# Optimization experiments

Hardware: AMD Instinct MI355X
Metric: run time of the kernel (lower is better)

## Reference

```python
import jax, jax.numpy as jnp
import numpy as np

DIM = 1024
NUM_HEADS = 16
HEAD_DIM = DIM // NUM_HEADS
MLP_DIM = 4 * DIM
EPS = 1e-5


def layer_norm(x, g, b):
    mu = jnp.mean(x, axis=-1, keepdims=True)
    var = jnp.mean(jnp.square(x - mu), axis=-1, keepdims=True)
    return (x - mu) * jax.lax.rsqrt(var + EPS) * g + b


def setup_inputs() -> dict:
    key = jax.random.key(0)
    ks = jax.random.split(key, 12)
    B, L = 2, 2048
    s = lambda n: 1.0 / np.sqrt(n)
    return {
        "x": jax.random.normal(ks[0], (B, L, DIM), jnp.float32),
        "attn_mask": jnp.tril(jnp.ones((L, L), jnp.int32))[None, None],  # [1,1,L,L]
        "w_qkv": jax.random.normal(ks[1], (DIM, 3 * DIM), jnp.float32) * s(DIM),
        "b_qkv": jnp.zeros((3 * DIM,), jnp.float32),
        "w_proj": jax.random.normal(ks[2], (DIM, DIM), jnp.float32) * s(DIM),
        "b_proj": jnp.zeros((DIM,), jnp.float32),
        "w_fc1": jax.random.normal(ks[3], (DIM, MLP_DIM), jnp.float32) * s(DIM),
        "b_fc1": jnp.zeros((MLP_DIM,), jnp.float32),
        "w_fc2": jax.random.normal(ks[4], (MLP_DIM, DIM), jnp.float32) * s(MLP_DIM),
        "b_fc2": jnp.zeros((DIM,), jnp.float32),
        "g1": jnp.ones((DIM,), jnp.float32),
        "beta1": jnp.zeros((DIM,), jnp.float32),
        "g2": jnp.ones((DIM,), jnp.float32),
        "beta2": jnp.zeros((DIM,), jnp.float32),
    }


def reference(x, attn_mask, w_qkv, b_qkv, w_proj, b_proj, w_fc1, b_fc1,
              w_fc2, b_fc2, g1, beta1, g2, beta2):
    B, L, D = x.shape
    scale = HEAD_DIM ** -0.5

    # --- attention branch (pre-norm) ---
    h = layer_norm(x, g1, beta1)
    qkv = h @ w_qkv + b_qkv                                  # [B,L,3D]
    qkv = qkv.reshape(B, L, 3, NUM_HEADS, HEAD_DIM)
    q = qkv[:, :, 0].transpose(0, 2, 1, 3)                   # [B,H,L,hd]
    k = qkv[:, :, 1].transpose(0, 2, 1, 3)
    v = qkv[:, :, 2].transpose(0, 2, 1, 3)
    attn = jnp.einsum('bhqd,bhkd->bhqk', q, k) * scale       # [B,H,L,L]
    attn = jnp.where(attn_mask == 0, -jnp.inf, attn)
    attn = jax.nn.softmax(attn, axis=-1)
    y = jnp.einsum('bhqk,bhkd->bhqd', attn, v)               # [B,H,L,hd]
    y = y.transpose(0, 2, 1, 3).reshape(B, L, D)
    y = y @ w_proj + b_proj
    x = x + y

    # --- MLP branch (pre-norm) ---
    h = layer_norm(x, g2, beta2)
    h = jax.nn.gelu(h @ w_fc1 + b_fc1, approximate=False)
    h = h @ w_fc2 + b_fc2
    return x + h
```

## Files before the change

kernel.cpp:

```cpp
#include <hip/hip_runtime.h>
#include <hip/hip_bf16.h>
#include <stdint.h>

typedef unsigned short u16;
typedef __attribute__((ext_vector_type(8))) short bf16x8;
typedef __attribute__((ext_vector_type(4))) float f32x4;
typedef __attribute__((ext_vector_type(16))) float f32x16;
typedef __attribute__((ext_vector_type(4))) unsigned short u16x4;

#define DEVI static __device__ __forceinline__

DEVI u16 f2bf(float f) {
    unsigned int u = __builtin_bit_cast(unsigned int, f);
    return (u16)((u + 0x7fffu + ((u >> 16) & 1u)) >> 16);
}

DEVI float gelu_f(float v) {
    const float z = 1.5957691216f * (v + 0.044715f * v * v * v);
    return v / (1.0f + __expf(-z));
}

DEVI void async_copy16(const void* g, void* l) {
    __builtin_amdgcn_global_load_lds((const __attribute__((address_space(1))) void*)g,
                                     (__attribute__((address_space(3))) void*)l,
                                     16, 0, 0);
}

__global__ __launch_bounds__(256) void tcvt_kernel(const float* __restrict__ src,
                                                   u16* __restrict__ dst,
                                                   int K, int N) {
    __shared__ float tile[32][33];
    const int k0 = blockIdx.x * 32, n0 = blockIdx.y * 32;
    const int t = threadIdx.x;
    const int c = t & 31, r0 = t >> 5;
#pragma unroll
    for (int p = 0; p < 4; ++p) {
        const int r = r0 + p * 8;
        tile[r][c] = src[(size_t)(k0 + r) * N + n0 + c];
    }
    __syncthreads();
#pragma unroll
    for (int p = 0; p < 4; ++p) {
        const int r = r0 + p * 8;
        dst[(size_t)(n0 + r) * K + k0 + c] = f2bf(tile[c][r]);
    }
}

__global__ __launch_bounds__(256) void ln_kernel(const float* __restrict__ x,
                                                 const float* __restrict__ gw,
                                                 const float* __restrict__ bw,
                                                 u16* __restrict__ out) {
    const int row = blockIdx.x;
    const int t = threadIdx.x;
    const float4 v = ((const float4*)(x + (size_t)row * 1024))[t];
    float s  = v.x + v.y + v.z + v.w;
    float ss = v.x * v.x + v.y * v.y + v.z * v.z + v.w * v.w;
#pragma unroll
    for (int off = 32; off > 0; off >>= 1) {
        s  += __shfl_down(s, off);
        ss += __shfl_down(ss, off);
    }
    __shared__ float red[8];
    const int wv = t >> 6;
    if ((t & 63) == 0) { red[wv] = s; red[4 + wv] = ss; }
    __syncthreads();
    if (t == 0) {
        red[0] = red[0] + red[1] + red[2] + red[3];
        red[4] = red[4] + red[5] + red[6] + red[7];
    }
    __syncthreads();
    const float mean = red[0] * (1.0f / 1024.0f);
    const float var  = red[4] * (1.0f / 1024.0f) - mean * mean;
    const float rstd = rsqrtf(var + 1e-5f);
    const float4 gv = ((const float4*)gw)[t];
    const float4 bv = ((const float4*)bw)[t];
    u16x4 o;
    o[0] = f2bf((v.x - mean) * rstd * gv.x + bv.x);
    o[1] = f2bf((v.y - mean) * rstd * gv.y + bv.y);
    o[2] = f2bf((v.z - mean) * rstd * gv.z + bv.z);
    o[3] = f2bf((v.w - mean) * rstd * gv.w + bv.w);
    ((u16x4*)out)[(size_t)row * 256 + t] = o;
}

DEVI void stage64(const char* g, size_t ldb, char* lds0, int lane, int wv) {
    const int colsw = ((lane & 3) << 4) ^ (lane & 32);
    const int rl = lane >> 2;
#pragma unroll
    for (int i = 0; i < 4; ++i) {
        const int s = wv * 4 + i;
        const int kh = s >> 3, c = s & 7;
        async_copy16(g + (size_t)(c * 16 + rl) * ldb + kh * 64 + colsw,
                     lds0 + s * 1024);
    }
}

template <int EPI, int SPLITK>
__global__ __launch_bounds__(256, 4) void gemmv6(const u16* __restrict__ A,
                                                 const u16* __restrict__ Bt,
                                                 const float* __restrict__ bias,
                                                 void* __restrict__ out0,
                                                 void* __restrict__ out1,
                                                 void* __restrict__ out2,
                                                 int M, int N, int K) {
    __shared__ __align__(16) char As[16384];
    __shared__ __align__(16) char Bs[16384];
    const int tid = threadIdx.x;
    const int lane = tid & 63, wv = tid >> 6;
    const int wr = wv >> 1, wc = wv & 1;
    const int g = lane >> 4, qq = lane & 15;
    const int rdoff = qq * 64 + ((g * 16) ^ ((qq & 8) << 2));

    const int nwg = gridDim.x;
    int id = blockIdx.x;
    id = (id & 7) * (nwg >> 3) + (id >> 3);
    const int MT = M >> 7, NTn = N >> 7;
    const int slice = id / (MT * NTn);
    const int r2 = id % (MT * NTn);
    const int m0 = (r2 % MT) << 7;
    const int n0 = (r2 / MT) << 7;
    const int Ks = K / SPLITK;
    const int NT = Ks >> 6;
    const size_t ldb = (size_t)K * 2;

    const char* pa = (const char*)A + (size_t)m0 * ldb + (size_t)slice * Ks * 2;
    const char* pb = (const char*)Bt + (size_t)n0 * ldb + (size_t)slice * Ks * 2;

    f32x4 acc[4][4] = {};

    for (int t = 0; t < NT; ++t) {
        stage64(pa + (size_t)t * 128, ldb, As, lane, wv);
        stage64(pb + (size_t)t * 128, ldb, Bs, lane, wv);
        __syncthreads();
#pragma unroll
        for (int kh = 0; kh < 2; ++kh) {
            bf16x8 fa[4], fb[4];
#pragma unroll
            for (int fn = 0; fn < 4; ++fn)
                fb[fn] = *(const bf16x8*)(Bs + (kh * 8 + wc * 4 + fn) * 1024 + rdoff);
#pragma unroll
            for (int fm = 0; fm < 4; ++fm)
                fa[fm] = *(const bf16x8*)(As + (kh * 8 + wr * 4 + fm) * 1024 + rdoff);
#pragma unroll
            for (int fm = 0; fm < 4; ++fm)
#pragma unroll
                for (int fn = 0; fn < 4; ++fn)
                    acc[fm][fn] = __builtin_amdgcn_mfma_f32_16x16x32_bf16(fa[fm], fb[fn],
                                                                          acc[fm][fn], 0, 0, 0);
        }
        __syncthreads();
    }

#pragma unroll
    for (int fm = 0; fm < 4; ++fm) {
#pragma unroll
        for (int fn = 0; fn < 4; ++fn) {
            const int mrow = m0 + wr * 64 + fm * 16 + g * 4;
            const int ncol = n0 + wc * 64 + fn * 16 + qq;
            if constexpr (EPI == 0) {
                const float bs = bias[ncol];
                const int sec = ncol >> 10;
                const int hd_ = ncol & 1023;
                const int hh = hd_ >> 6, dd = hd_ & 63;
                if (sec == 2) {
                    const int b_ = mrow >> 11, l_ = mrow & 2047;
                    u16x4 pk;
#pragma unroll
                    for (int r = 0; r < 4; ++r) pk[r] = f2bf(acc[fm][fn][r] + bs);
                    *(u16x4*)((u16*)out2 + ((size_t)((b_ * 16 + hh) * 64 + dd)) * 2048 + l_) = pk;
                } else {
                    u16* dst = (sec == 0) ? (u16*)out0 : (u16*)out1;
                    const float sc = (sec == 0) ? 0.1803368801f : 1.0f;
#pragma unroll
                    for (int r = 0; r < 4; ++r) {
                        const int mr = mrow + r;
                        const int b_ = mr >> 11, l_ = mr & 2047;
                        dst[((size_t)((b_ * 16 + hh) * 2048 + l_)) * 64 + dd] =
                            f2bf((acc[fm][fn][r] + bs) * sc);
                    }
                }
            } else if constexpr (EPI == 2) {
                const float bs = bias[ncol];
                u16* dst = (u16*)out0;
#pragma unroll
                for (int r = 0; r < 4; ++r)
                    dst[(size_t)(mrow + r) * N + ncol] = f2bf(gelu_f(acc[fm][fn][r] + bs));
            } else {
                float* dst = (float*)out0 + (size_t)slice * M * N;
#pragma unroll
                for (int r = 0; r < 4; ++r)
                    dst[(size_t)(mrow + r) * N + ncol] = acc[fm][fn][r];
            }
        }
    }
}

template <int SPLIT>
__global__ __launch_bounds__(256) void reduceN_kernel(const float* __restrict__ p,
                                                      const float* __restrict__ bias,
                                                      const float* __restrict__ res,
                                                      float* __restrict__ out,
                                                      int MN4, int N4) {
    const int i = blockIdx.x * 256 + threadIdx.x;
    float4 s = ((const float4*)p)[i];
#pragma unroll
    for (int s2 = 1; s2 < SPLIT; ++s2) {
        const float4 q = ((const float4*)p)[(size_t)s2 * MN4 + i];
        s.x += q.x; s.y += q.y; s.z += q.z; s.w += q.w;
    }
    const float4 r = ((const float4*)res)[i];
    const float4 bs = ((const float4*)bias)[i & (N4 - 1)];
    float4 o;
    o.x = s.x + r.x + bs.x;
    o.y = s.y + r.y + bs.y;
    o.z = s.z + r.z + bs.z;
    o.w = s.w + r.w + bs.w;
    ((float4*)out)[i] = o;
}

DEVI void stage_kv(const char* kbase, const char* vbase, int key0,
                   u16* ksm, u16* vsm, int wv, int lane) {
#pragma unroll
    for (int i = 0; i < 2; ++i) {
        const int c = wv + i * 4;
        const int off = c * 1024 + lane * 16;
        const int row = off >> 7;
        const int scol = (off & 127) ^ ((row & 7) << 4);
        async_copy16(kbase + (size_t)key0 * 128 + (size_t)row * 128 + scol,
                     (char*)ksm + c * 1024);
    }
#pragma unroll
    for (int i = 0; i < 2; ++i) {
        const int c = wv + i * 4;
        const int row = c * 8 + (lane >> 3);
        const int scol = ((lane & 7) * 16) ^ ((row & 7) << 4);
        async_copy16(vbase + (size_t)row * 4096 + (size_t)key0 * 2 + scol,
                     (char*)vsm + c * 1024);
    }
}

__global__ __launch_bounds__(256, 3) void attn32_kernel(const u16* __restrict__ Q,
                                                        const u16* __restrict__ Kk,
                                                        const u16* __restrict__ Vt,
                                                        u16* __restrict__ Y) {
    const int bh = blockIdx.y;
    const int b_ = bh >> 4, hh = bh & 15;
    const int qb = gridDim.x - 1 - blockIdx.x;
    const int tid = threadIdx.x;
    const int wv = tid >> 6, lane = tid & 63;
    const int hi = lane >> 5, qc = lane & 31;

    __shared__ __align__(16) u16 Ksm[2][4096];
    __shared__ __align__(16) u16 Vsm[2][4096];
    __shared__ __align__(16) u16 Pl[4][32 * 72];

    const char* Kb = (const char*)(Kk + (size_t)bh * 2048 * 64);
    const char* Vb = (const char*)(Vt + (size_t)bh * 64 * 2048);
    u16* Pw = &Pl[wv][0];
    const u16* Pr = Pw + qc * 72;

    const int q0w = qb * 128 + wv * 32;
    const int qg = q0w + qc;
    const int ntile = qb * 2 + 2;
    const int ntile_w = qb * 2 + (wv >> 1) + 1;

    bf16x8 qf[4];
    {
        const u16* Qp = Q + ((size_t)bh * 2048 + q0w + qc) * 64;
#pragma unroll
        for (int c = 0; c < 4; ++c)
            qf[c] = *(const bf16x8*)(Qp + c * 16 + hi * 8);
    }

    f32x16 oacc[2];
#pragma unroll
    for (int r = 0; r < 16; ++r) { oacc[0][r] = 0.0f; oacc[1][r] = 0.0f; }
    float m_run = -1e30f, l_run = 0.0f;

    stage_kv(Kb, Vb, 0, Ksm[0], Vsm[0], wv, lane);
    __syncthreads();
    int cur = 0;
    for (int kt = 0; kt < ntile; ++kt) {
        const int key0 = kt * 64;
        if (kt + 1 < ntile)
            stage_kv(Kb, Vb, key0 + 64, Ksm[cur ^ 1], Vsm[cur ^ 1], wv, lane);
        if (kt < ntile_w) {
            f32x16 sacc[2];
#pragma unroll
            for (int r = 0; r < 16; ++r) { sacc[0][r] = 0.0f; sacc[1][r] = 0.0f; }
#pragma unroll
            for (int c = 0; c < 4; ++c) {
#pragma unroll
                for (int kb = 0; kb < 2; ++kb) {
                    const int kr = kb * 32 + qc;
                    const bf16x8 ak = *(const bf16x8*)((const char*)Ksm[cur] + kr * 128 +
                                          ((c * 32 + hi * 16) ^ ((kr & 7) << 4)));
                    sacc[kb] = __builtin_amdgcn_mfma_f32_32x32x16_bf16(ak, qf[c],
                                                                       sacc[kb], 0, 0, 0);
                }
            }
            float pmax = -1e30f;
            if (key0 + 63 > q0w) {
#pragma unroll
                for (int kb = 0; kb < 2; ++kb)
#pragma unroll
                    for (int r = 0; r < 16; ++r) {
                        const int key = key0 + kb * 32 + (r & 3) + 8 * (r >> 2) + 4 * hi;
                        float s = sacc[kb][r];
                        if (key > qg) s = -1e30f;
                        sacc[kb][r] = s;
                        pmax = fmaxf(pmax, s);
                    }
            } else {
#pragma unroll
                for (int kb = 0; kb < 2; ++kb)
#pragma unroll
                    for (int r = 0; r < 16; ++r) pmax = fmaxf(pmax, sacc[kb][r]);
            }
            pmax = fmaxf(pmax, __shfl_xor(pmax, 32));
            if (pmax > m_run + 11.0f) {
                const float alpha = __builtin_amdgcn_exp2f(m_run - pmax);
#pragma unroll
                for (int r = 0; r < 16; ++r) { oacc[0][r] *= alpha; oacc[1][r] *= alpha; }
                l_run *= alpha;
                m_run = pmax;
            }
            float lsum = 0.0f;
#pragma unroll
            for (int kb = 0; kb < 2; ++kb)
#pragma unroll
                for (int j = 0; j < 4; ++j) {
                    u16x4 pk4;
#pragma unroll
                    for (int t = 0; t < 4; ++t) {
                        const float e = __builtin_amdgcn_exp2f(sacc[kb][j * 4 + t] - m_run);
                        lsum += e;
                        pk4[t] = f2bf(e);
                    }
                    *(u16x4*)(Pw + qc * 72 + kb * 32 + j * 8 + 4 * hi) = pk4;
                }
            lsum += __shfl_xor(lsum, 32);
            l_run += lsum;
#pragma unroll
            for (int c = 0; c < 4; ++c) {
                const bf16x8 pf = *(const bf16x8*)(Pr + c * 16 + hi * 8);
#pragma unroll
                for (int db = 0; db < 2; ++db) {
                    const int dr = db * 32 + qc;
                    const bf16x8 av = *(const bf16x8*)((const char*)Vsm[cur] + dr * 128 +
                                          ((c * 32 + hi * 16) ^ ((dr & 7) << 4)));
                    oacc[db] = __builtin_amdgcn_mfma_f32_32x32x16_bf16(av, pf,
                                                                       oacc[db], 0, 0, 0);
                }
            }
        }
        __syncthreads();
        cur ^= 1;
    }
    const float inv = 1.0f / l_run;
    u16* Yp = &Y[((size_t)(b_ * 2048 + qg)) * 1024 + hh * 64];
#pragma unroll
    for (int db = 0; db < 2; ++db)
#pragma unroll
        for (int j = 0; j < 4; ++j) {
            u16x4 o;
#pragma unroll
            for (int t = 0; t < 4; ++t) o[t] = f2bf(oacc[db][j * 4 + t] * inv);
            *(u16x4*)(Yp + db * 32 + j * 8 + 4 * hi) = o;
        }
}

extern "C" void kernel_launch(void* const* d_in, const int* in_sizes, int n_in,
                              void* d_out, int out_size, void* d_ws, size_t ws_size,
                              hipStream_t stream) {
    (void)in_sizes; (void)n_in; (void)out_size;
    const float* x      = (const float*)d_in[0];
    const float* w_qkv  = (const float*)d_in[2];
    const float* b_qkv  = (const float*)d_in[3];
    const float* w_proj = (const float*)d_in[4];
    const float* b_proj = (const float*)d_in[5];
    const float* w_fc1  = (const float*)d_in[6];
    const float* b_fc1  = (const float*)d_in[7];
    const float* w_fc2  = (const float*)d_in[8];
    const float* b_fc2  = (const float*)d_in[9];
    const float* g1     = (const float*)d_in[10];
    const float* be1    = (const float*)d_in[11];
    const float* g2     = (const float*)d_in[12];
    const float* be2    = (const float*)d_in[13];

    char* ws = (char*)d_ws;
    size_t off = 0;
    auto alloc = [&](size_t bytes) { size_t r = off; off += (bytes + 255) & ~(size_t)255; return r; };
    u16*   wt_qkv = (u16*)(ws + alloc((size_t)3072 * 1024 * 2));
    u16*   wt_prj = (u16*)(ws + alloc((size_t)1024 * 1024 * 2));
    u16*   wt_fc1 = (u16*)(ws + alloc((size_t)4096 * 1024 * 2));
    u16*   wt_fc2 = (u16*)(ws + alloc((size_t)1024 * 4096 * 2));
    u16*   hbuf   = (u16*)(ws + alloc((size_t)4096 * 1024 * 2));
    float* x1     = (float*)(ws + alloc((size_t)4096 * 1024 * 4));
    char*  big    = ws + alloc((size_t)33554432);
    u16* qb  = (u16*)(big);
    u16* kb  = (u16*)(big + 8388608);
    u16* vtb = (u16*)(big + 16777216);
    u16* yb  = (u16*)(big + 25165824);
    u16* act = (u16*)(big);
    if (off > ws_size) return;
    const size_t part_need = (size_t)4 * 4096 * 1024 * 4;
    if ((ws_size - off) < part_need) return;
    float* part = (float*)(ws + off);

    const dim3 blk(256);
    tcvt_kernel<<<dim3(32, 96), blk, 0, stream>>>(w_qkv, wt_qkv, 1024, 3072);
    tcvt_kernel<<<dim3(32, 32), blk, 0, stream>>>(w_proj, wt_prj, 1024, 1024);
    tcvt_kernel<<<dim3(32, 128), blk, 0, stream>>>(w_fc1, wt_fc1, 1024, 4096);
    tcvt_kernel<<<dim3(128, 32), blk, 0, stream>>>(w_fc2, wt_fc2, 4096, 1024);

    ln_kernel<<<dim3(4096), blk, 0, stream>>>(x, g1, be1, hbuf);
    gemmv6<0, 1><<<dim3(768), blk, 0, stream>>>(hbuf, wt_qkv, b_qkv,
                                                qb, kb, vtb, 4096, 3072, 1024);
    attn32_kernel<<<dim3(16, 32), blk, 0, stream>>>(qb, kb, vtb, yb);
    gemmv6<4, 2><<<dim3(512), blk, 0, stream>>>(yb, wt_prj, nullptr,
                                                part, nullptr, nullptr, 4096, 1024, 1024);
    reduceN_kernel<2><<<dim3(4096), blk, 0, stream>>>(part, b_proj, x, x1, 1048576, 256);
    ln_kernel<<<dim3(4096), blk, 0, stream>>>(x1, g2, be2, hbuf);
    gemmv6<2, 1><<<dim3(1024), blk, 0, stream>>>(hbuf, wt_fc1, b_fc1,
                                                 act, nullptr, nullptr, 4096, 4096, 1024);
    gemmv6<4, 4><<<dim3(1024), blk, 0, stream>>>(act, wt_fc2, nullptr,
                                                 part, nullptr, nullptr, 4096, 1024, 4096);
    reduceN_kernel<4><<<dim3(4096), blk, 0, stream>>>(part, b_fc2, x1, (float*)d_out,
                                                      1048576, 256);
}
```

Measured before the change: 254.1 us.

## Split causal attention over two key segments with a separate combine kernel

The attention kernel now splits each query block's key range into two halves, launched as separate blocks along a new grid dimension. Each half writes unnormalized fp32 partial outputs plus running max and sum to workspace. A new combine kernel merges the two halves with exp2 rescaling and writes the bf16 result. The intent is to double block-level parallelism and shorten the long causal tail of late query blocks, at the cost of extra fp32 partial traffic and one more kernel launch.

```diff
diff --git a/kernel.cpp b/kernel.cpp
--- a/kernel.cpp
+++ b/kernel.cpp
@@ -238,12 +238,13 @@
     }
 }
 
-__global__ __launch_bounds__(256, 3) void attn32_kernel(const u16* __restrict__ Q,
-                                                        const u16* __restrict__ Kk,
-                                                        const u16* __restrict__ Vt,
-                                                        u16* __restrict__ Y) {
-    const int bh = blockIdx.y;
-    const int b_ = bh >> 4, hh = bh & 15;
+__global__ __launch_bounds__(256, 3) void attn32_seg(const u16* __restrict__ Q,
+                                                     const u16* __restrict__ Kk,
+                                                     const u16* __restrict__ Vt,
+                                                     float* __restrict__ opart,
+                                                     float2* __restrict__ ml) {
+    const int bh = blockIdx.z;
+    const int seg = blockIdx.y;
     const int qb = gridDim.x - 1 - blockIdx.x;
     const int tid = threadIdx.x;
     const int wv = tid >> 6, lane = tid & 63;
@@ -260,12 +261,14 @@
 
     const int q0w = qb * 128 + wv * 32;
     const int qg = q0w + qc;
-    const int ntile = qb * 2 + 2;
-    const int ntile_w = qb * 2 + (wv >> 1) + 1;
+    const int nt_half = qb + 1;
+    const int kt_begin = seg ? nt_half : 0;
+    const int kt_end = seg ? (2 * qb + 2) : nt_half;
+    const int ntw = min(kt_end, 2 * qb + (wv >> 1) + 1);
 
     bf16x8 qf[4];
     {
-        const u16* Qp = Q + ((size_t)bh * 2048 + q0w + qc) * 64;
+        const u16* Qp = Q + ((size_t)bh * 2048 + qg) * 64;
 #pragma unroll
         for (int c = 0; c < 4; ++c)
             qf[c] = *(const bf16x8*)(Qp + c * 16 + hi * 8);
@@ -274,16 +277,16 @@
     f32x16 oacc[2];
 #pragma unroll
     for (int r = 0; r < 16; ++r) { oacc[0][r] = 0.0f; oacc[1][r] = 0.0f; }
-    float m_run = -1e30f, l_run = 0.0f;
-
-    stage_kv(Kb, Vb, 0, Ksm[0], Vsm[0], wv, lane);
+    float m_run = -60000.0f, l_run = 0.0f;
+
+    stage_kv(Kb, Vb, kt_begin * 64, Ksm[0], Vsm[0], wv, lane);
     __syncthreads();
     int cur = 0;
-    for (int kt = 0; kt < ntile; ++kt) {
+    for (int kt = kt_begin; kt < kt_end; ++kt) {
         const int key0 = kt * 64;
-        if (kt + 1 < ntile)
+        if (kt + 1 < kt_end)
             stage_kv(Kb, Vb, key0 + 64, Ksm[cur ^ 1], Vsm[cur ^ 1], wv, lane);
-        if (kt < ntile_w) {
+        if (kt < ntw) {
             f32x16 sacc[2];
 #pragma unroll
             for (int r = 0; r < 16; ++r) { sacc[0][r] = 0.0f; sacc[1][r] = 0.0f; }
@@ -356,17 +359,44 @@
         __syncthreads();
         cur ^= 1;
     }
-    const float inv = 1.0f / l_run;
-    u16* Yp = &Y[((size_t)(b_ * 2048 + qg)) * 1024 + hh * 64];
+
+    const size_t row = (size_t)seg * 65536 + (size_t)bh * 2048 + qg;
+    float* op = opart + row * 64;
 #pragma unroll
     for (int db = 0; db < 2; ++db)
 #pragma unroll
         for (int j = 0; j < 4; ++j) {
-            u16x4 o;
-#pragma unroll
-            for (int t = 0; t < 4; ++t) o[t] = f2bf(oacc[db][j * 4 + t] * inv);
-            *(u16x4*)(Yp + db * 32 + j * 8 + 4 * hi) = o;
+            float4 v;
+            v.x = oacc[db][j * 4 + 0];
+            v.y = oacc[db][j * 4 + 1];
+            v.z = oacc[db][j * 4 + 2];
+            v.w = oacc[db][j * 4 + 3];
+            *(float4*)(op + db * 32 + j * 8 + 4 * hi) = v;
         }
+    if (hi == 0) { float2 t; t.x = m_run; t.y = l_run; ml[row] = t; }
+}
+
+__global__ __launch_bounds__(256) void attn_comb(const float* __restrict__ opart,
+                                                 const float2* __restrict__ ml,
+                                                 u16* __restrict__ Y) {
+    const int idx = blockIdx.x * 256 + threadIdx.x;
+    const int row = idx >> 4, d4 = idx & 15;
+    const float2 ml0 = ml[row];
+    const float2 ml1 = ml[65536 + row];
+    const float m = fmaxf(ml0.x, ml1.x);
+    const float w0 = __builtin_amdgcn_exp2f(ml0.x - m);
+    const float w1 = __builtin_amdgcn_exp2f(ml1.x - m);
+    const float inv = 1.0f / (ml0.y * w0 + ml1.y * w1);
+    const float4 a = ((const float4*)opart)[(size_t)row * 16 + d4];
+    const float4 b = ((const float4*)opart)[(size_t)(65536 + row) * 16 + d4];
+    const int bh = row >> 11, q = row & 2047;
+    const int b_ = bh >> 4, hh = bh & 15;
+    u16x4 o;
+    o[0] = f2bf((a.x * w0 + b.x * w1) * inv);
+    o[1] = f2bf((a.y * w0 + b.y * w1) * inv);
+    o[2] = f2bf((a.z * w0 + b.z * w1) * inv);
+    o[3] = f2bf((a.w * w0 + b.w * w1) * inv);
+    *(u16x4*)(Y + ((size_t)(b_ * 2048 + q)) * 1024 + hh * 64 + d4 * 4) = o;
 }
 
 extern "C" void kernel_launch(void* const* d_in, const int* in_sizes, int n_in,
@@ -403,9 +433,11 @@
     u16* yb  = (u16*)(big + 25165824);
     u16* act = (u16*)(big);
     if (off > ws_size) return;
-    const size_t part_need = (size_t)4 * 4096 * 1024 * 4;
+    const size_t part_need = (size_t)4 * 4096 * 1024 * 4 + (size_t)2 * 65536 * 8;
     if ((ws_size - off) < part_need) return;
-    float* part = (float*)(ws + off);
+    float*  part  = (float*)(ws + off);
+    float*  opart = part;
+    float2* mlp   = (float2*)(ws + off + (size_t)4 * 4096 * 1024 * 4);
 
     const dim3 blk(256);
     tcvt_kernel<<<dim3(32, 96), blk, 0, stream>>>(w_qkv, wt_qkv, 1024, 3072);
@@ -416,7 +448,8 @@
     ln_kernel<<<dim3(4096), blk, 0, stream>>>(x, g1, be1, hbuf);
     gemmv6<0, 1><<<dim3(768), blk, 0, stream>>>(hbuf, wt_qkv, b_qkv,
                                                 qb, kb, vtb, 4096, 3072, 1024);
-    attn32_kernel<<<dim3(16, 32), blk, 0, stream>>>(qb, kb, vtb, yb);
+    attn32_seg<<<dim3(16, 2, 32), blk, 0, stream>>>(qb, kb, vtb, opart, mlp);
+    attn_comb<<<dim3(4096), blk, 0, stream>>>(opart, mlp, yb);
     gemmv6<4, 2><<<dim3(512), blk, 0, stream>>>(yb, wt_prj, nullptr,
                                                 part, nullptr, nullptr, 4096, 1024, 1024);
     reduceN_kernel<2><<<dim3(4096), blk, 0, stream>>>(part, b_proj, x, x1, 1048576, 256);
```

Result: slower. 261.5 us (+2.9%).
